# Optimization experiments

Measured on AMD Instinct MI355X. Metric: run time of the kernel, lower is better.

The kernel has to match this reference:

```python
import jax, jax.numpy as jnp
import numpy as np

N, E = 50000, 800000
IN_C, HID_C, OUT_C = 256, 256, 256


def setup_inputs() -> dict:
    key = jax.random.key(0)
    ks = jax.random.split(key, 8)
    x_piece = jax.random.normal(ks[0], (N, IN_C), dtype=jnp.float32)
    edge_index_piece = jax.random.randint(ks[1], (2, E), 0, N, dtype=jnp.int64)
    batch = jnp.zeros((N,), dtype=jnp.int64)
    def glorot(k, fan_in, fan_out):
        s = jnp.sqrt(6.0 / (fan_in + fan_out)).astype(jnp.float32)
        return jax.random.uniform(k, (fan_in, fan_out), jnp.float32, -s, s)
    return {
        "x_piece": x_piece,
        "edge_index_piece": edge_index_piece,
        "batch": batch,
        "W1": glorot(ks[2], IN_C, HID_C), "b1": jnp.zeros((HID_C,), jnp.float32),
        "W2": glorot(ks[3], HID_C, HID_C), "b2": jnp.zeros((HID_C,), jnp.float32),
        "W3": glorot(ks[4], HID_C, OUT_C), "b3": jnp.zeros((OUT_C,), jnp.float32),
    }


def _gcn_prep(edge_index, n_nodes):
    # add self-loops, compute symmetric normalization (PyG GCNConv default)
    src = jnp.concatenate([edge_index[0], jnp.arange(n_nodes, dtype=edge_index.dtype)])
    dst = jnp.concatenate([edge_index[1], jnp.arange(n_nodes, dtype=edge_index.dtype)])
    deg = jax.ops.segment_sum(jnp.ones_like(dst, dtype=jnp.float32), dst, num_segments=n_nodes)
    deg_inv_sqrt = jnp.where(deg > 0, jax.lax.rsqrt(jnp.maximum(deg, 1.0)), 0.0)
    norm = deg_inv_sqrt[src] * deg_inv_sqrt[dst]  # [E+N]
    return src, dst, norm


def _gcn_layer(x, src, dst, norm, W, b, n_nodes):
    h = x @ W                                   # [N, out] dense transform first
    msg = h[src] * norm[:, None]                # gather + scale
    out = jax.ops.segment_sum(msg, dst, num_segments=n_nodes)  # scatter-add
    return out + b


def reference(x_piece, edge_index_piece, batch, W1, b1, W2, b2, W3, b3):
    n_nodes = x_piece.shape[0]
    src, dst, norm = _gcn_prep(edge_index_piece, n_nodes)
    x = _gcn_layer(x_piece, src, dst, norm, W1, b1, n_nodes)
    x = jax.nn.gelu(x)
    x = _gcn_layer(x, src, dst, norm, W2, b2, n_nodes)
    x = jax.nn.gelu(x)
    x = _gcn_layer(x, src, dst, norm, W3, b3, n_nodes)
    return x
```

## Files before the change

### kernel.cpp

```cpp
#include <hip/hip_runtime.h>
#include <cstdint>
#include <cstddef>

#define CH 256

typedef _Float16 f16x8 __attribute__((ext_vector_type(8)));
typedef _Float16 f16x4 __attribute__((ext_vector_type(4)));
typedef float f32x4 __attribute__((ext_vector_type(4)));
typedef short short8 __attribute__((ext_vector_type(8)));

#define GLOB(x) ((const __attribute__((address_space(1))) void*)(x))
#define LDSP(x) ((__attribute__((address_space(3))) void*)(x))


__device__ __forceinline__ int ld_idx(const void* p, long long i, int w64) {
    if (w64) return (int)((const long long*)p)[i];
    return ((const int*)p)[i];
}

__device__ __forceinline__ float gelu_f(float x) {
    float x3 = x * x * x;
    float t = tanhf(0.7978845608028654f * (x + 0.044715f * x3));
    return 0.5f * x * (1.0f + t);
}


__global__ void k_detect(const void* __restrict__ ei, int* __restrict__ flag, int E) {
    int l = threadIdx.x;
    long long k = ((long long)l * (long long)(E - 1)) / 63;
    int w = ((const int*)ei)[2 * k + 1];
    unsigned long long vote = __ballot(w == 0);
    if (l == 0) *flag = (vote == ~0ULL) ? 1 : 0;
}

__global__ void k_deg(const void* __restrict__ ei, const int* __restrict__ flag,
                      int* __restrict__ deg, int E) {
    int e = blockIdx.x * blockDim.x + threadIdx.x;
    if (e >= E) return;
    int w64 = *flag;
    int d = ld_idx(ei, (long long)E + e, w64);
    atomicAdd(&deg[d], 1);
}

__global__ void k_dis(const int* __restrict__ deg, float* __restrict__ dis, int N) {
    int n = blockIdx.x * blockDim.x + threadIdx.x;
    if (n >= N) return;
    dis[n] = 1.0f / sqrtf((float)(deg[n] + 1));
}

__global__ void k_scan_block(const int* __restrict__ deg, int* __restrict__ rowptr,
                             int* __restrict__ partial, int N) {
    __shared__ int s[256];
    int gid = blockIdx.x * 256 + threadIdx.x;
    int v = (gid < N) ? deg[gid] : 0;
    s[threadIdx.x] = v;
    __syncthreads();
    for (int off = 1; off < 256; off <<= 1) {
        int t = (threadIdx.x >= off) ? s[threadIdx.x - off] : 0;
        __syncthreads();
        s[threadIdx.x] += t;
        __syncthreads();
    }
    if (gid < N) rowptr[gid] = s[threadIdx.x] - v;
    if (threadIdx.x == 255) partial[blockIdx.x] = s[255];
}

__global__ void k_scan_partial(int* __restrict__ partial, int nb) {
    __shared__ int s[256];
    int i = threadIdx.x;
    int v = (i < nb) ? partial[i] : 0;
    s[i] = v;
    __syncthreads();
    for (int off = 1; off < 256; off <<= 1) {
        int t = (i >= off) ? s[i - off] : 0;
        __syncthreads();
        s[i] += t;
        __syncthreads();
    }
    if (i < nb) partial[i] = s[i] - v;
}

__global__ void k_add_off(int* __restrict__ rowptr, const int* __restrict__ partial,
                          int N, int E) {
    int gid = blockIdx.x * 256 + threadIdx.x;
    if (gid < N) rowptr[gid] += partial[blockIdx.x];
    if (gid == 0) rowptr[N] = E;
}

__global__ void k_scatter(const void* __restrict__ ei, const int* __restrict__ flag,
                          const float* __restrict__ dis, const int* __restrict__ rowptr,
                          int* __restrict__ cnt, int2* __restrict__ epack, int E) {
    int e = blockIdx.x * blockDim.x + threadIdx.x;
    if (e >= E) return;
    int w64 = *flag;
    int s = ld_idx(ei, e, w64);
    int d = ld_idx(ei, (long long)E + e, w64);
    int pos = rowptr[d] + atomicAdd(&cnt[d], 1);
    epack[pos] = make_int2(s, __float_as_int(dis[s] * dis[d]));
}


__global__ void k_split_w(const float* __restrict__ W, _Float16* __restrict__ Wh) {
    int k = threadIdx.x;
    int c = blockIdx.x;
    Wh[c * CH + k] = (_Float16)W[k * CH + c];
}


__global__ __launch_bounds__(256) void k_quant_x(const float* __restrict__ x,
                                                 uint8_t* __restrict__ Xout,
                                                 float* __restrict__ sout, int N) {
    int node = blockIdx.x * 4 + threadIdx.y;
    if (node >= N) return;
    int lane = threadIdx.x;
    float4 v = ((const float4*)(x + (size_t)node * CH))[lane];
    float mx = fmaxf(fmaxf(fabsf(v.x), fabsf(v.y)), fmaxf(fabsf(v.z), fabsf(v.w)));
    #pragma unroll
    for (int off = 32; off > 0; off >>= 1)
        mx = fmaxf(mx, __shfl_xor(mx, off));
    float inv = (mx > 0.f) ? (32767.0f / mx) : 0.f;
    short4 q;
    q.x = (short)__float2int_rn(v.x * inv);
    q.y = (short)__float2int_rn(v.y * inv);
    q.z = (short)__float2int_rn(v.z * inv);
    q.w = (short)__float2int_rn(v.w * inv);
    *(short4*)(Xout + (size_t)node * 512 + (size_t)lane * 8) = q;
    if (lane == 0) sout[node] = mx * (1.0f / 32767.0f);
}


#define GM 128
#define GN 128
#define GK 32

__global__ __launch_bounds__(256, 2)
void k_gemm16(const uint8_t* __restrict__ X16, const float* __restrict__ sx,
              const _Float16* __restrict__ Bh,
              uint8_t* __restrict__ H16, float* __restrict__ scales, int M) {
    __shared__ __align__(16) char smem[65536];
    short*    lA16 = (short*)smem;
    _Float16* lB   = (_Float16*)(smem + 16384);

    const int tid  = threadIdx.x;
    const int lane = tid & 63;
    const int wid  = tid >> 6;
    const int m0   = blockIdx.x * GM;
    const int n0   = blockIdx.y * GN;
    const int wm   = wid >> 1, wn = wid & 1;
    const int r15  = lane & 15, kg = lane >> 4;

    auto stage = [&](int buf, int k0) {
        #pragma unroll
        for (int c = 0; c < 4; c++) {
            int call = wid * 4 + c;
            int cc = call & 7;
            int L = cc * 64 + lane;
            int row = L >> 2, ch = L & 3;
            int sch = ch ^ ((row >> 1) & 3);
            if (call < 8) {
                int gr = m0 + row; gr = (gr < M) ? gr : (M - 1);
                const uint8_t* g = X16 + (size_t)gr * 512 + (size_t)k0 * 2 + (sch << 4);
                __builtin_amdgcn_global_load_lds(GLOB(g), LDSP(&lA16[buf * 4096 + L * 8]), 16, 0, 0);
            } else {
                const _Float16* g = Bh + (size_t)(n0 + row) * CH + k0 + (sch << 3);
                __builtin_amdgcn_global_load_lds(GLOB(g), LDSP(&lB[buf * 4096 + L * 8]), 16, 0, 0);
            }
        }
    };

    f32x4 acc[4][4];
    #pragma unroll
    for (int i = 0; i < 4; i++)
        #pragma unroll
        for (int n = 0; n < 4; n++)
            acc[i][n] = (f32x4){0.f, 0.f, 0.f, 0.f};

    stage(0, 0);
    __syncthreads();

    for (int ks = 0; ks < 8; ks++) {
        int cur = ks & 1;
        if (ks < 7) stage(cur ^ 1, (ks + 1) * GK);

        f16x8 aq[4], bh[4];
        #pragma unroll
        for (int i = 0; i < 4; i++) {
            int R = wm * 64 + i * 16 + r15;
            int p = kg ^ ((R >> 1) & 3);
            short8 q = *(const short8*)&lA16[cur * 4096 + R * 32 + p * 8];
            #pragma unroll
            for (int j = 0; j < 8; j++)
                aq[i][j] = (_Float16)q[j];
        }
        #pragma unroll
        for (int n = 0; n < 4; n++) {
            int C = wn * 64 + n * 16 + r15;
            int p = kg ^ ((C >> 1) & 3);
            bh[n] = *(const f16x8*)&lB[cur * 4096 + C * GK + p * 8];
        }
        #pragma unroll
        for (int i = 0; i < 4; i++)
            #pragma unroll
            for (int n = 0; n < 4; n++)
                acc[i][n] = __builtin_amdgcn_mfma_f32_16x16x32_f16(aq[i], bh[n], acc[i][n], 0, 0, 0);
        __syncthreads();
    }

    float sC[4][4];
    #pragma unroll
    for (int i = 0; i < 4; i++)
        #pragma unroll
        for (int r = 0; r < 4; r++) {
            int gr = m0 + wm * 64 + i * 16 + kg * 4 + r;
            sC[i][r] = sx[(gr < M) ? gr : (M - 1)];
        }
    #pragma unroll
    for (int i = 0; i < 4; i++)
        #pragma unroll
        for (int n = 0; n < 4; n++)
            #pragma unroll
            for (int r = 0; r < 4; r++)
                acc[i][n][r] *= sC[i][r];

    float mx = 0.f;
    #pragma unroll
    for (int i = 0; i < 4; i++)
        #pragma unroll
        for (int n = 0; n < 4; n++)
            #pragma unroll
            for (int r = 0; r < 4; r++)
                mx = fmaxf(mx, fabsf(acc[i][n][r]));
    #pragma unroll
    for (int off = 32; off > 0; off >>= 1)
        mx = fmaxf(mx, __shfl_xor(mx, off));
    if (lane == 0) ((float*)smem)[wid] = mx;
    __syncthreads();
    float tmax = fmaxf(fmaxf(((float*)smem)[0], ((float*)smem)[1]),
                       fmaxf(((float*)smem)[2], ((float*)smem)[3]));
    float scl = tmax * (1.0f / 32767.0f);
    float inv = (tmax > 0.f) ? (32767.0f / tmax) : 0.f;
    __syncthreads();

    float* ep = (float*)smem + wid * 4096;
    #pragma unroll
    for (int i = 0; i < 4; i++)
        #pragma unroll
        for (int n = 0; n < 4; n++)
            #pragma unroll
            for (int r = 0; r < 4; r++)
                ep[(i * 16 + kg * 4 + r) * 64 + n * 16 + r15] = acc[i][n][r];
    __syncthreads();

    int q = lane & 15;
    int rsub = lane >> 4;
    #pragma unroll
    for (int p = 0; p < 16; p++) {
        int lrow = p * 4 + rsub;
        int grow = m0 + wm * 64 + lrow;
        if (grow < M) {
            int q0 = __float2int_rn(ep[lrow * 64 + q * 4 + 0] * inv);
            int q1 = __float2int_rn(ep[lrow * 64 + q * 4 + 1] * inv);
            int q2 = __float2int_rn(ep[lrow * 64 + q * 4 + 2] * inv);
            int q3 = __float2int_rn(ep[lrow * 64 + q * 4 + 3] * inv);
            uint2 d;
            d.x = (q0 & 0xFFFF) | (q1 << 16);
            d.y = (q2 & 0xFFFF) | (q3 << 16);
            int col = n0 + wn * 64 + q * 4;
            *(uint2*)(H16 + (size_t)grow * 512 + (size_t)col * 2) = d;
        }
    }

    if (tid < GM && m0 + tid < M) scales[(size_t)(m0 + tid) * 2 + (n0 >> 7)] = scl;
}


template <int MODE>
__global__ __launch_bounds__(256) void k_agg(const uint8_t* __restrict__ H16,
                                             const float* __restrict__ scales,
                                             const float* __restrict__ dis,
                                             const int* __restrict__ rowptr,
                                             const int2* __restrict__ epack,
                                             const float* __restrict__ bias,
                                             float* __restrict__ out,
                                             uint8_t* __restrict__ Xout,
                                             float* __restrict__ sxout, int N) {
    int node = blockIdx.x * 4 + threadIdx.y;
    if (node >= N) return;
    int lane = threadIdx.x;
    int half = lane >> 5;
    float d = dis[node];
    short4 hv = *(const short4*)(H16 + (size_t)node * 512 + (size_t)lane * 8);
    float wself = d * d * scales[(size_t)node * 2 + half];
    float ax = wself * (float)hv.x, ay = wself * (float)hv.y;
    float az = wself * (float)hv.z, aw = wself * (float)hv.w;
    int s = rowptr[node], e = rowptr[node + 1];
    int j = s;
    for (; j + 8 <= e; j += 8) {
        int2 p[8];
        #pragma unroll
        for (int t = 0; t < 8; t++) p[t] = epack[j + t];
        short4 v[8];
        float sc[8];
        #pragma unroll
        for (int t = 0; t < 8; t++) {
            v[t] = *(const short4*)(H16 + (size_t)p[t].x * 512 + (size_t)lane * 8);
            sc[t] = scales[(size_t)p[t].x * 2 + half];
        }
        #pragma unroll
        for (int t = 0; t < 8; t++) {
            float wn = __int_as_float(p[t].y) * sc[t];
            ax += wn * (float)v[t].x; ay += wn * (float)v[t].y;
            az += wn * (float)v[t].z; aw += wn * (float)v[t].w;
        }
    }
    for (; j < e; j++) {
        int2 p = epack[j];
        float wn = __int_as_float(p.y) * scales[(size_t)p.x * 2 + half];
        short4 v = *(const short4*)(H16 + (size_t)p.x * 512 + (size_t)lane * 8);
        ax += wn * (float)v.x; ay += wn * (float)v.y;
        az += wn * (float)v.z; aw += wn * (float)v.w;
    }
    float4 b = ((const float4*)bias)[lane];
    ax += b.x; ay += b.y; az += b.z; aw += b.w;
    if (MODE == 0) {
        ax = gelu_f(ax); ay = gelu_f(ay); az = gelu_f(az); aw = gelu_f(aw);
        float mx = fmaxf(fmaxf(fabsf(ax), fabsf(ay)), fmaxf(fabsf(az), fabsf(aw)));
        #pragma unroll
        for (int off = 32; off > 0; off >>= 1)
            mx = fmaxf(mx, __shfl_xor(mx, off));
        float inv = (mx > 0.f) ? (32767.0f / mx) : 0.f;
        short4 q;
        q.x = (short)__float2int_rn(ax * inv);
        q.y = (short)__float2int_rn(ay * inv);
        q.z = (short)__float2int_rn(az * inv);
        q.w = (short)__float2int_rn(aw * inv);
        *(short4*)(Xout + (size_t)node * 512 + (size_t)lane * 8) = q;
        if (lane == 0) sxout[node] = mx * (1.0f / 32767.0f);
    } else {
        ((float4*)(out + (size_t)node * CH))[lane] = make_float4(ax, ay, az, aw);
    }
}


extern "C" void kernel_launch(void* const* d_in, const int* in_sizes, int n_in,
                              void* d_out, int out_size, void* d_ws, size_t ws_size,
                              hipStream_t stream) {
    const float* x  = (const float*)d_in[0];
    const void*  ei = d_in[1];
    const float* W1 = (const float*)d_in[3]; const float* b1 = (const float*)d_in[4];
    const float* W2 = (const float*)d_in[5]; const float* b2 = (const float*)d_in[6];
    const float* W3 = (const float*)d_in[7]; const float* b3 = (const float*)d_in[8];

    int N = in_sizes[0] / CH;
    int E = in_sizes[1] / 2;
    float* out = (float*)d_out;

    char* ws = (char*)d_ws;
    auto take = [&](size_t bytes) {
        char* p = ws;
        ws += (bytes + 15) & ~(size_t)15;
        return p;
    };
    uint8_t*  H16    = (uint8_t*) take((size_t)N * 512);
    uint8_t*  Xa     = (uint8_t*) take((size_t)N * 512);
    uint8_t*  Xb     = (uint8_t*) take((size_t)N * 512);
    float*    hscl   = (float*)   take((size_t)N * 2 * sizeof(float));
    float*    sxa    = (float*)   take((size_t)N * sizeof(float));
    float*    sxb    = (float*)   take((size_t)N * sizeof(float));
    int*      deg    = (int*)     take((size_t)N * sizeof(int));
    float*    dis    = (float*)   take((size_t)N * sizeof(float));
    int*      rowptr = (int*)     take((size_t)(N + 1) * sizeof(int));
    int*      cnt    = (int*)     take((size_t)N * sizeof(int));
    int*      part   = (int*)     take(4096);
    int*      flag   = (int*)     take(16);
    int2*     epack  = (int2*)    take((size_t)E * sizeof(int2));
    _Float16* Wh1    = (_Float16*)take((size_t)CH * CH * 2);
    _Float16* Wh2    = (_Float16*)take((size_t)CH * CH * 2);
    _Float16* Wh3    = (_Float16*)take((size_t)CH * CH * 2);

    hipMemsetAsync(deg, 0, (size_t)N * sizeof(int), stream);
    hipMemsetAsync(cnt, 0, (size_t)N * sizeof(int), stream);

    int eb = (E + 255) / 256;
    int nb = (N + 255) / 256;

    k_detect<<<1, 64, 0, stream>>>(ei, flag, E);
    k_deg<<<eb, 256, 0, stream>>>(ei, flag, deg, E);
    k_dis<<<nb, 256, 0, stream>>>(deg, dis, N);
    k_scan_block<<<nb, 256, 0, stream>>>(deg, rowptr, part, N);
    k_scan_partial<<<1, 256, 0, stream>>>(part, nb);
    k_add_off<<<nb, 256, 0, stream>>>(rowptr, part, N, E);
    k_scatter<<<eb, 256, 0, stream>>>(ei, flag, dis, rowptr, cnt, epack, E);

    k_split_w<<<CH, CH, 0, stream>>>(W1, Wh1);
    k_split_w<<<CH, CH, 0, stream>>>(W2, Wh2);
    k_split_w<<<CH, CH, 0, stream>>>(W3, Wh3);

    dim3 qgrid((N + 3) / 4);
    dim3 qblock(64, 4);
    k_quant_x<<<qgrid, qblock, 0, stream>>>(x, Xa, sxa, N);

    dim3 ggrid((N + GM - 1) / GM, CH / GN);
    dim3 agrid((N + 3) / 4);
    dim3 ablock(64, 4);

    k_gemm16<<<ggrid, 256, 0, stream>>>(Xa, sxa, Wh1, H16, hscl, N);
    k_agg<0><<<agrid, ablock, 0, stream>>>(H16, hscl, dis, rowptr, epack, b1, out, Xb, sxb, N);
    k_gemm16<<<ggrid, 256, 0, stream>>>(Xb, sxb, Wh2, H16, hscl, N);
    k_agg<0><<<agrid, ablock, 0, stream>>>(H16, hscl, dis, rowptr, epack, b2, out, Xa, sxa, N);
    k_gemm16<<<ggrid, 256, 0, stream>>>(Xa, sxa, Wh3, H16, hscl, N);
    k_agg<1><<<agrid, ablock, 0, stream>>>(H16, hscl, dis, rowptr, epack, b3, out, Xb, sxb, N);
}
```

Measured before the change: 389.9 us.

## Fold source normalization into GEMM scales and shrink CSR edges to int indices

The per-edge norm dis[s]*dis[d] is split: the GEMM epilogue multiplies each row's quantization scale by dis[row], and aggregation multiplies by the destination's dis. The CSR edge array then stores only int source indices instead of int2 pairs, halving edge-stream reads in all three aggregations. The dis computation is fused into the scan offset kernel, and the three weight-conversion launches are merged into one. The cost is an extra dis read in the GEMM epilogue and a per-edge multiply by d.

```diff
diff --git a/kernel.cpp b/kernel.cpp
--- a/kernel.cpp
+++ b/kernel.cpp
@@ -42,12 +42,6 @@
     atomicAdd(&deg[d], 1);
 }
 
-__global__ void k_dis(const int* __restrict__ deg, float* __restrict__ dis, int N) {
-    int n = blockIdx.x * blockDim.x + threadIdx.x;
-    if (n >= N) return;
-    dis[n] = 1.0f / sqrtf((float)(deg[n] + 1));
-}
-
 __global__ void k_scan_block(const int* __restrict__ deg, int* __restrict__ rowptr,
                              int* __restrict__ partial, int N) {
     __shared__ int s[256];
@@ -81,26 +75,34 @@
 }
 
 __global__ void k_add_off(int* __restrict__ rowptr, const int* __restrict__ partial,
+                          const int* __restrict__ deg, float* __restrict__ dis,
                           int N, int E) {
     int gid = blockIdx.x * 256 + threadIdx.x;
-    if (gid < N) rowptr[gid] += partial[blockIdx.x];
+    if (gid < N) {
+        rowptr[gid] += partial[blockIdx.x];
+        dis[gid] = 1.0f / sqrtf((float)(deg[gid] + 1));
+    }
     if (gid == 0) rowptr[N] = E;
 }
 
 __global__ void k_scatter(const void* __restrict__ ei, const int* __restrict__ flag,
-                          const float* __restrict__ dis, const int* __restrict__ rowptr,
-                          int* __restrict__ cnt, int2* __restrict__ epack, int E) {
+                          const int* __restrict__ rowptr, int* __restrict__ cnt,
+                          int* __restrict__ ssrc, int E) {
     int e = blockIdx.x * blockDim.x + threadIdx.x;
     if (e >= E) return;
     int w64 = *flag;
     int s = ld_idx(ei, e, w64);
     int d = ld_idx(ei, (long long)E + e, w64);
     int pos = rowptr[d] + atomicAdd(&cnt[d], 1);
-    epack[pos] = make_int2(s, __float_as_int(dis[s] * dis[d]));
-}
-
-
-__global__ void k_split_w(const float* __restrict__ W, _Float16* __restrict__ Wh) {
+    ssrc[pos] = s;
+}
+
+
+__global__ void k_split_w3(const float* __restrict__ W1, const float* __restrict__ W2,
+                           const float* __restrict__ W3, _Float16* __restrict__ Wh1,
+                           _Float16* __restrict__ Wh2, _Float16* __restrict__ Wh3) {
+    const float* W = (blockIdx.y == 0) ? W1 : (blockIdx.y == 1) ? W2 : W3;
+    _Float16*   Wh = (blockIdx.y == 0) ? Wh1 : (blockIdx.y == 1) ? Wh2 : Wh3;
     int k = threadIdx.x;
     int c = blockIdx.x;
     Wh[c * CH + k] = (_Float16)W[k * CH + c];
@@ -135,8 +137,8 @@
 
 __global__ __launch_bounds__(256, 2)
 void k_gemm16(const uint8_t* __restrict__ X16, const float* __restrict__ sx,
-              const _Float16* __restrict__ Bh,
-              uint8_t* __restrict__ H16, float* __restrict__ scales, int M) {
+              const _Float16* __restrict__ Bh, const float* __restrict__ dis,
+              uint8_t* __restrict__ H16, float* __restrict__ hcomb, int M) {
     __shared__ __align__(16) char smem[65536];
     short*    lA16 = (short*)smem;
     _Float16* lB   = (_Float16*)(smem + 16384);
@@ -270,16 +272,17 @@
         }
     }
 
-    if (tid < GM && m0 + tid < M) scales[(size_t)(m0 + tid) * 2 + (n0 >> 7)] = scl;
+    if (tid < GM && m0 + tid < M)
+        hcomb[(size_t)(m0 + tid) * 2 + (n0 >> 7)] = scl * dis[m0 + tid];
 }
 
 
 template <int MODE>
 __global__ __launch_bounds__(256) void k_agg(const uint8_t* __restrict__ H16,
-                                             const float* __restrict__ scales,
+                                             const float* __restrict__ hcomb,
                                              const float* __restrict__ dis,
                                              const int* __restrict__ rowptr,
-                                             const int2* __restrict__ epack,
+                                             const int* __restrict__ ssrc,
                                              const float* __restrict__ bias,
                                              float* __restrict__ out,
                                              uint8_t* __restrict__ Xout,
@@ -290,33 +293,33 @@
     int half = lane >> 5;
     float d = dis[node];
     short4 hv = *(const short4*)(H16 + (size_t)node * 512 + (size_t)lane * 8);
-    float wself = d * d * scales[(size_t)node * 2 + half];
+    float wself = d * hcomb[(size_t)node * 2 + half];
     float ax = wself * (float)hv.x, ay = wself * (float)hv.y;
     float az = wself * (float)hv.z, aw = wself * (float)hv.w;
     int s = rowptr[node], e = rowptr[node + 1];
     int j = s;
     for (; j + 8 <= e; j += 8) {
-        int2 p[8];
-        #pragma unroll
-        for (int t = 0; t < 8; t++) p[t] = epack[j + t];
+        int p[8];
+        #pragma unroll
+        for (int t = 0; t < 8; t++) p[t] = ssrc[j + t];
         short4 v[8];
         float sc[8];
         #pragma unroll
         for (int t = 0; t < 8; t++) {
-            v[t] = *(const short4*)(H16 + (size_t)p[t].x * 512 + (size_t)lane * 8);
-            sc[t] = scales[(size_t)p[t].x * 2 + half];
+            v[t] = *(const short4*)(H16 + (size_t)p[t] * 512 + (size_t)lane * 8);
+            sc[t] = hcomb[(size_t)p[t] * 2 + half];
         }
         #pragma unroll
         for (int t = 0; t < 8; t++) {
-            float wn = __int_as_float(p[t].y) * sc[t];
+            float wn = d * sc[t];
             ax += wn * (float)v[t].x; ay += wn * (float)v[t].y;
             az += wn * (float)v[t].z; aw += wn * (float)v[t].w;
         }
     }
     for (; j < e; j++) {
-        int2 p = epack[j];
-        float wn = __int_as_float(p.y) * scales[(size_t)p.x * 2 + half];
-        short4 v = *(const short4*)(H16 + (size_t)p.x * 512 + (size_t)lane * 8);
+        int p = ssrc[j];
+        float wn = d * hcomb[(size_t)p * 2 + half];
+        short4 v = *(const short4*)(H16 + (size_t)p * 512 + (size_t)lane * 8);
         ax += wn * (float)v.x; ay += wn * (float)v.y;
         az += wn * (float)v.z; aw += wn * (float)v.w;
     }
@@ -364,7 +367,7 @@
     uint8_t*  H16    = (uint8_t*) take((size_t)N * 512);
     uint8_t*  Xa     = (uint8_t*) take((size_t)N * 512);
     uint8_t*  Xb     = (uint8_t*) take((size_t)N * 512);
-    float*    hscl   = (float*)   take((size_t)N * 2 * sizeof(float));
+    float*    hcomb  = (float*)   take((size_t)N * 2 * sizeof(float));
     float*    sxa    = (float*)   take((size_t)N * sizeof(float));
     float*    sxb    = (float*)   take((size_t)N * sizeof(float));
     int*      deg    = (int*)     take((size_t)N * sizeof(int));
@@ -373,7 +376,7 @@
     int*      cnt    = (int*)     take((size_t)N * sizeof(int));
     int*      part   = (int*)     take(4096);
     int*      flag   = (int*)     take(16);
-    int2*     epack  = (int2*)    take((size_t)E * sizeof(int2));
+    int*      ssrc   = (int*)     take((size_t)E * sizeof(int));
     _Float16* Wh1    = (_Float16*)take((size_t)CH * CH * 2);
     _Float16* Wh2    = (_Float16*)take((size_t)CH * CH * 2);
     _Float16* Wh3    = (_Float16*)take((size_t)CH * CH * 2);
@@ -386,15 +389,13 @@
 
     k_detect<<<1, 64, 0, stream>>>(ei, flag, E);
     k_deg<<<eb, 256, 0, stream>>>(ei, flag, deg, E);
-    k_dis<<<nb, 256, 0, stream>>>(deg, dis, N);
     k_scan_block<<<nb, 256, 0, stream>>>(deg, rowptr, part, N);
     k_scan_partial<<<1, 256, 0, stream>>>(part, nb);
-    k_add_off<<<nb, 256, 0, stream>>>(rowptr, part, N, E);
-    k_scatter<<<eb, 256, 0, stream>>>(ei, flag, dis, rowptr, cnt, epack, E);
-
-    k_split_w<<<CH, CH, 0, stream>>>(W1, Wh1);
-    k_split_w<<<CH, CH, 0, stream>>>(W2, Wh2);
-    k_split_w<<<CH, CH, 0, stream>>>(W3, Wh3);
+    k_add_off<<<nb, 256, 0, stream>>>(rowptr, part, deg, dis, N, E);
+    k_scatter<<<eb, 256, 0, stream>>>(ei, flag, rowptr, cnt, ssrc, E);
+
+    dim3 wgrid(CH, 3);
+    k_split_w3<<<wgrid, CH, 0, stream>>>(W1, W2, W3, Wh1, Wh2, Wh3);
 
     dim3 qgrid((N + 3) / 4);
     dim3 qblock(64, 4);
@@ -404,10 +405,10 @@
     dim3 agrid((N + 3) / 4);
     dim3 ablock(64, 4);
 
-    k_gemm16<<<ggrid, 256, 0, stream>>>(Xa, sxa, Wh1, H16, hscl, N);
-    k_agg<0><<<agrid, ablock, 0, stream>>>(H16, hscl, dis, rowptr, epack, b1, out, Xb, sxb, N);
-    k_gemm16<<<ggrid, 256, 0, stream>>>(Xb, sxb, Wh2, H16, hscl, N);
-    k_agg<0><<<agrid, ablock, 0, stream>>>(H16, hscl, dis, rowptr, epack, b2, out, Xa, sxa, N);
-    k_gemm16<<<ggrid, 256, 0, stream>>>(Xa, sxa, Wh3, H16, hscl, N);
-    k_agg<1><<<agrid, ablock, 0, stream>>>(H16, hscl, dis, rowptr, epack, b3, out, Xb, sxb, N);
-}
+    k_gemm16<<<ggrid, 256, 0, stream>>>(Xa, sxa, Wh1, dis, H16, hcomb, N);
+    k_agg<0><<<agrid, ablock, 0, stream>>>(H16, hcomb, dis, rowptr, ssrc, b1, out, Xb, sxb, N);
+    k_gemm16<<<ggrid, 256, 0, stream>>>(Xb, sxb, Wh2, dis, H16, hcomb, N);
+    k_agg<0><<<agrid, ablock, 0, stream>>>(H16, hcomb, dis, rowptr, ssrc, b2, out, Xa, sxa, N);
+    k_gemm16<<<ggrid, 256, 0, stream>>>(Xa, sxa, Wh3, dis, H16, hcomb, N);
+    k_agg<1><<<agrid, ablock, 0, stream>>>(H16, hcomb, dis, rowptr, ssrc, b3, out, Xb, sxb, N);
+}
```

New measurement: 385.6 us. No clear change (-1.1%).
